# Optimization experiments

Measured on AMD Instinct MI355X. Metric: run time of the kernel, lower is better.

## Reference

```python
import jax, jax.numpy as jnp
import numpy as np

B, V, S, H = 16384, 16, 64, 512


def setup_inputs() -> dict:
    key = jax.random.key(0)
    kx, kw, kb, kws, kbs = jax.random.split(key, 5)
    x = jax.random.normal(kx, (B, V, S), dtype=jnp.float32)
    # per-variable linear layers: weight [V, S, H], bias [V, H]
    W = jax.random.normal(kw, (V, S, H), dtype=jnp.float32) * (1.0 / np.sqrt(S))
    b = jax.random.normal(kb, (V, H), dtype=jnp.float32) * 0.01
    # variable selection linear: hidden -> V
    W_sel = jax.random.normal(kws, (H, V), dtype=jnp.float32) * (1.0 / np.sqrt(H))
    b_sel = jax.random.normal(kbs, (V,), dtype=jnp.float32) * 0.01
    return {"x": x, "W": W, "b": b, "W_sel": W_sel, "b_sel": b_sel}


def reference(x, W, b, W_sel, b_sel):
    # per-variable linears: [B, V, H]
    transformed = jnp.einsum('bvs,vsh->bvh', x, W) + b  # grouped small GEMMs
    # torch stacks to [B, H, V]; mean over variable axis -> [B, H]
    flat = transformed.mean(axis=1)
    # softmax-gated selection weights [B, V] (dropout is identity in eval)
    weights = jax.nn.softmax(flat @ W_sel + b_sel, axis=-1)
    # weighted sum over variables -> [B, H]
    out = jnp.einsum('bvh,bv->bh', transformed, weights)
    return out
```

## Files before the change

kernel.cpp:

```cpp
#include <hip/hip_runtime.h>
#include <hip/hip_bf16.h>
#include <stdint.h>

#define B_ROWS 16384
#define VDIM   16
#define SDIM   64
#define HDIM   512
#define KDIM   1024
#define KP     1056
#define ASTR   1064
#define MROWS  32
#define PLOG_OFF 68096
#define WLDS_OFF (68096 + 8704)
#define K2_LDS   (68096 + 8704 + 2048)

using bf16x8 = __attribute__((ext_vector_type(8))) __bf16;
using u16x8  = __attribute__((ext_vector_type(8))) unsigned short;
using f32x4  = __attribute__((ext_vector_type(4))) float;

__device__ __forceinline__ unsigned short f2bf(float f) {
  unsigned int u = __builtin_bit_cast(unsigned int, f);
  u = (u + 0x7FFFu + ((u >> 16) & 1u)) >> 16;
  return (unsigned short)u;
}
__device__ __forceinline__ float bf2f(unsigned short s) {
  return __builtin_bit_cast(float, (unsigned int)s << 16);
}

__global__ __launch_bounds__(256) void k0_prep(
    const float* __restrict__ W, const float* __restrict__ bias,
    const float* __restrict__ Wsel, const float* __restrict__ bsel,
    unsigned short* __restrict__ Bt, unsigned short* __restrict__ WcombT,
    float* __restrict__ bcomb) {
  __shared__ float bm[HDIM];
  __shared__ float part[16][17];
  __shared__ unsigned short tile[32][264];
  const int t = threadIdx.x;
  if (blockIdx.x < 66) {
    const int k0 = (blockIdx.x >> 1) * 32;
    const int n  = ((blockIdx.x & 1) << 8) + t;
    #pragma unroll 8
    for (int kk = 0; kk < 32; ++kk) {
      const int k = k0 + kk;
      float val;
      if (k < KDIM)            val = W[(size_t)k * HDIM + n];
      else if (k < KDIM + 16)  val = bias[(size_t)(k - KDIM) * HDIM + n];
      else                     val = 0.f;
      tile[kk][t] = f2bf(val);
    }
    __syncthreads();
    unsigned short* dst = Bt + (size_t)n * KP + k0;
    #pragma unroll
    for (int seg = 0; seg < 4; ++seg) {
      unsigned short o[8];
      #pragma unroll
      for (int jj = 0; jj < 8; ++jj) o[jj] = tile[seg * 8 + jj][t];
      *(u16x8*)(dst + seg * 8) = *(const u16x8*)o;
    }
    return;
  }
  const int bid = blockIdx.x - 66;
  if (bid < 256) {
    const int wave = t >> 6, lane = t & 63;
    const int k = bid * 4 + wave;
    const float* wr = W + (size_t)k * HDIM;
    float s[16];
    #pragma unroll
    for (int v = 0; v < 16; ++v) s[v] = 0.f;
    #pragma unroll
    for (int j = 0; j < 8; ++j) {
      const int h = lane + 64 * j;
      const float a = wr[h];
      const float4* wl = (const float4*)(Wsel + h * 16);
      const float4 q0 = wl[0], q1 = wl[1], q2 = wl[2], q3 = wl[3];
      s[0]  = fmaf(a, q0.x, s[0]);  s[1]  = fmaf(a, q0.y, s[1]);
      s[2]  = fmaf(a, q0.z, s[2]);  s[3]  = fmaf(a, q0.w, s[3]);
      s[4]  = fmaf(a, q1.x, s[4]);  s[5]  = fmaf(a, q1.y, s[5]);
      s[6]  = fmaf(a, q1.z, s[6]);  s[7]  = fmaf(a, q1.w, s[7]);
      s[8]  = fmaf(a, q2.x, s[8]);  s[9]  = fmaf(a, q2.y, s[9]);
      s[10] = fmaf(a, q2.z, s[10]); s[11] = fmaf(a, q2.w, s[11]);
      s[12] = fmaf(a, q3.x, s[12]); s[13] = fmaf(a, q3.y, s[13]);
      s[14] = fmaf(a, q3.z, s[14]); s[15] = fmaf(a, q3.w, s[15]);
    }
    #pragma unroll
    for (int off = 32; off > 0; off >>= 1) {
      #pragma unroll
      for (int v = 0; v < 16; ++v) s[v] += __shfl_xor(s[v], off, 64);
    }
    float mine = 0.f;
    #pragma unroll
    for (int v = 0; v < 16; ++v) mine = (lane == v) ? s[v] : mine;
    if (lane < 16) WcombT[lane * KDIM + k] = f2bf(mine * (1.f / 16.f));
  } else {
    for (int h = t; h < HDIM; h += 256) {
      float s = 0.f;
      #pragma unroll
      for (int v = 0; v < VDIM; ++v) s += bias[v * HDIM + h];
      bm[h] = s * (1.f / 16.f);
    }
    __syncthreads();
    int v = t & 15, sl = t >> 4;
    float s = 0.f;
    for (int h = sl * 32; h < sl * 32 + 32; ++h) s = fmaf(bm[h], Wsel[h * VDIM + v], s);
    part[sl][v] = s;
    __syncthreads();
    if (t < 16) {
      float s2 = bsel[t];
      #pragma unroll
      for (int i = 0; i < 16; ++i) s2 += part[i][t];
      bcomb[t] = s2;
    }
  }
}

__global__ __launch_bounds__(512, 4) void k2f_fused(
    const float* __restrict__ x, const unsigned short* __restrict__ WcombT,
    const float* __restrict__ bcomb, const unsigned short* __restrict__ Bt,
    float* __restrict__ C) {
  extern __shared__ unsigned short As[];
  float* plog = (float*)((char*)As + PLOG_OFF);
  float* wlds = (float*)((char*)As + WLDS_OFF);

  const int t = threadIdx.x;
  const int rowb = blockIdx.x * MROWS;
  const int wave = t >> 6, lane = t & 63;
  const int mlane = lane & 15, quad = lane >> 4;

  const int srow = t >> 4;
  const int sc = (t & 15) * 8;
  u16x8 xreg[8];
  {
    const float* xr = x + (size_t)(rowb + srow) * KDIM + sc;
    unsigned short* aw = As + srow * ASTR + sc;
    #pragma unroll
    for (int i = 0; i < 8; ++i) {
      const f32x4 a0 = __builtin_nontemporal_load((const f32x4*)(xr + i * 128));
      const f32x4 a1 = __builtin_nontemporal_load((const f32x4*)(xr + i * 128 + 4));
      u16x8 u;
      u[0] = f2bf(a0[0]); u[1] = f2bf(a0[1]); u[2] = f2bf(a0[2]); u[3] = f2bf(a0[3]);
      u[4] = f2bf(a1[0]); u[5] = f2bf(a1[1]); u[6] = f2bf(a1[2]); u[7] = f2bf(a1[3]);
      xreg[i] = u;
      *(u16x8*)(aw + i * 128) = u;
    }
  }
  __syncthreads();

  {
    const int kh = wave >> 1, rg = wave & 1;
    const unsigned short* al = As + (rg * 16 + mlane) * ASTR + kh * 256 + quad * 8;
    const unsigned short* bl = WcombT + mlane * KDIM + kh * 256 + quad * 8;
    f32x4 acc = {0.f, 0.f, 0.f, 0.f};
    #pragma unroll
    for (int kt = 0; kt < 8; ++kt) {
      bf16x8 a = *(const bf16x8*)al; al += 32;
      bf16x8 b = *(const bf16x8*)bl; bl += 32;
      acc = __builtin_amdgcn_mfma_f32_16x16x32_bf16(a, b, acc, 0, 0, 0);
    }
    float* pl = plog + ((size_t)((kh * 2 + rg) * 16 + quad * 4) * 17 + mlane);
    #pragma unroll
    for (int r = 0; r < 4; ++r) pl[r * 17] = acc[r];
  }
  __syncthreads();

  if (t < 32) {
    const int rg = t >> 4, rr = t & 15;
    float l[16];
    float mx = -1e30f;
    #pragma unroll
    for (int v = 0; v < 16; ++v) {
      float s = bcomb[v];
      #pragma unroll
      for (int kq = 0; kq < 4; ++kq)
        s += plog[((size_t)((kq * 2 + rg) * 16 + rr)) * 17 + v];
      l[v] = s;
      mx = fmaxf(mx, s);
    }
    float s = 0.f;
    #pragma unroll
    for (int v = 0; v < 16; ++v) { l[v] = __expf(l[v] - mx); s += l[v]; }
    const float inv = 1.f / s;
    float* wo = wlds + t * 16;
    #pragma unroll
    for (int v = 0; v < 16; ++v) wo[v] = l[v] * inv;
  }
  __syncthreads();

  {
    float wv[16];
    const f32x4* wq = (const f32x4*)(wlds + srow * 16);
    #pragma unroll
    for (int q = 0; q < 4; ++q) {
      const f32x4 f = wq[q];
      wv[4 * q + 0] = f[0]; wv[4 * q + 1] = f[1];
      wv[4 * q + 2] = f[2]; wv[4 * q + 3] = f[3];
    }
    const int vbase = (t & 15) >> 3;
    unsigned short* aw = As + srow * ASTR + sc;
    #pragma unroll
    for (int i = 0; i < 8; ++i) {
      const float w = wv[2 * i + vbase];
      const u16x8 a = xreg[i];
      u16x8 o;
      #pragma unroll
      for (int j = 0; j < 8; ++j) o[j] = f2bf(w * bf2f(a[j]));
      *(u16x8*)(aw + i * 128) = o;
    }
    if ((t & 15) < 4) {
      const int j8 = (t & 15) * 8;
      unsigned short o[8];
      #pragma unroll
      for (int jj = 0; jj < 8; ++jj)
        o[jj] = (j8 + jj < 16) ? f2bf(wv[j8 + jj]) : (unsigned short)0;
      *(u16x8*)(As + srow * ASTR + KDIM + j8) = *(const u16x8*)o;
    }
  }

  const int colb = wave * 64;
  const unsigned short* bp[4];
  #pragma unroll
  for (int j = 0; j < 4; ++j)
    bp[j] = Bt + (size_t)(colb + j * 16 + mlane) * KP + quad * 8;

  bf16x8 bv0[4], bv1[4];
  #pragma unroll
  for (int j = 0; j < 4; ++j) {
    bv0[j] = *(const bf16x8*)(bp[j]);
    bv1[j] = *(const bf16x8*)(bp[j] + 32);
    bp[j] += 64;
  }

  __syncthreads();

  const unsigned short* ap[2];
  #pragma unroll
  for (int i = 0; i < 2; ++i)
    ap[i] = As + (i * 16 + mlane) * ASTR + quad * 8;

  f32x4 acc[2][4];
  const f32x4 z = {0.f, 0.f, 0.f, 0.f};
  #pragma unroll
  for (int i = 0; i < 2; ++i)
    #pragma unroll
    for (int j = 0; j < 4; ++j) acc[i][j] = z;

  #pragma unroll 1
  for (int kt = 0; kt < 33; ++kt) {
    bf16x8 bnext[4];
    if (kt < 31) {
      #pragma unroll
      for (int j = 0; j < 4; ++j) { bnext[j] = *(const bf16x8*)bp[j]; bp[j] += 32; }
    }
    bf16x8 av[2];
    #pragma unroll
    for (int i = 0; i < 2; ++i) { av[i] = *(const bf16x8*)ap[i]; ap[i] += 32; }
    #pragma unroll
    for (int i = 0; i < 2; ++i)
      #pragma unroll
      for (int j = 0; j < 4; ++j)
        acc[i][j] = __builtin_amdgcn_mfma_f32_16x16x32_bf16(av[i], bv0[j], acc[i][j], 0, 0, 0);
    #pragma unroll
    for (int j = 0; j < 4; ++j) { bv0[j] = bv1[j]; bv1[j] = bnext[j]; }
  }

  #pragma unroll
  for (int i = 0; i < 2; ++i)
    #pragma unroll
    for (int j = 0; j < 4; ++j)
      #pragma unroll
      for (int r = 0; r < 4; ++r) {
        const size_t row = (size_t)rowb + i * 16 + quad * 4 + r;
        const int col = colb + j * 16 + mlane;
        __builtin_nontemporal_store(acc[i][j][r], &C[row * HDIM + col]);
      }
}

extern "C" void kernel_launch(void* const* d_in, const int* in_sizes, int n_in,
                              void* d_out, int out_size, void* d_ws, size_t ws_size,
                              hipStream_t stream) {
  const float* x    = (const float*)d_in[0];
  const float* W    = (const float*)d_in[1];
  const float* bias = (const float*)d_in[2];
  const float* Wsel = (const float*)d_in[3];
  const float* bsel = (const float*)d_in[4];
  float* out = (float*)d_out;

  char* ws = (char*)d_ws;
  unsigned short* Bt     = (unsigned short*)(ws);
  unsigned short* WcombT = (unsigned short*)(ws + 1081344);
  float*          bcomb  = (float*)(ws + 1114112);

  static int lds_set = 0;
  if (!lds_set) {
    hipFuncSetAttribute((const void*)k2f_fused,
                        hipFuncAttributeMaxDynamicSharedMemorySize, K2_LDS);
    lds_set = 1;
  }

  k0_prep<<<323, 256, 0, stream>>>(W, bias, Wsel, bsel, Bt, WcombT, bcomb);
  k2f_fused<<<512, 512, K2_LDS, stream>>>(x, WcombT, bcomb, Bt, out);
}
```

Before: 162.7 us.

## Split gate and GEMM into separate kernels with 64-row double-buffered tiles

```diff
diff --git a/kernel.cpp b/kernel.cpp
--- a/kernel.cpp
+++ b/kernel.cpp
@@ -8,14 +8,18 @@
 #define HDIM   512
 #define KDIM   1024
 #define KP     1056
-#define ASTR   1064
-#define MROWS  32
-#define PLOG_OFF 68096
-#define WLDS_OFF (68096 + 8704)
-#define K2_LDS   (68096 + 8704 + 2048)
+
+#define ASTR     1064
+#define G_PLOG   68096
+#define G_LDS    (68096 + 8704)
+
+#define CSTR     296
+#define BUFU16   (64 * CSTR)
+#define GEMM_LDS (2 * BUFU16 * 2)
 
 using bf16x8 = __attribute__((ext_vector_type(8))) __bf16;
 using u16x8  = __attribute__((ext_vector_type(8))) unsigned short;
+using u16x4  = __attribute__((ext_vector_type(4))) unsigned short;
 using f32x4  = __attribute__((ext_vector_type(4))) float;
 
 __device__ __forceinline__ unsigned short f2bf(float f) {
@@ -113,33 +117,29 @@
   }
 }
 
-__global__ __launch_bounds__(512, 4) void k2f_fused(
+__global__ __launch_bounds__(512, 4) void k1_gate(
     const float* __restrict__ x, const unsigned short* __restrict__ WcombT,
-    const float* __restrict__ bcomb, const unsigned short* __restrict__ Bt,
-    float* __restrict__ C) {
+    const float* __restrict__ bcomb, float* __restrict__ wgate) {
   extern __shared__ unsigned short As[];
-  float* plog = (float*)((char*)As + PLOG_OFF);
-  float* wlds = (float*)((char*)As + WLDS_OFF);
+  float* plog = (float*)((char*)As + G_PLOG);
 
   const int t = threadIdx.x;
-  const int rowb = blockIdx.x * MROWS;
+  const int rowb = blockIdx.x * 32;
   const int wave = t >> 6, lane = t & 63;
   const int mlane = lane & 15, quad = lane >> 4;
 
-  const int srow = t >> 4;
-  const int sc = (t & 15) * 8;
-  u16x8 xreg[8];
   {
+    const int srow = t >> 4;
+    const int sc = (t & 15) * 8;
     const float* xr = x + (size_t)(rowb + srow) * KDIM + sc;
     unsigned short* aw = As + srow * ASTR + sc;
     #pragma unroll
     for (int i = 0; i < 8; ++i) {
-      const f32x4 a0 = __builtin_nontemporal_load((const f32x4*)(xr + i * 128));
-      const f32x4 a1 = __builtin_nontemporal_load((const f32x4*)(xr + i * 128 + 4));
+      const float4 a0 = *(const float4*)(xr + i * 128);
+      const float4 a1 = *(const float4*)(xr + i * 128 + 4);
       u16x8 u;
-      u[0] = f2bf(a0[0]); u[1] = f2bf(a0[1]); u[2] = f2bf(a0[2]); u[3] = f2bf(a0[3]);
-      u[4] = f2bf(a1[0]); u[5] = f2bf(a1[1]); u[6] = f2bf(a1[2]); u[7] = f2bf(a1[3]);
-      xreg[i] = u;
+      u[0] = f2bf(a0.x); u[1] = f2bf(a0.y); u[2] = f2bf(a0.z); u[3] = f2bf(a0.w);
+      u[4] = f2bf(a1.x); u[5] = f2bf(a1.y); u[6] = f2bf(a1.z); u[7] = f2bf(a1.w);
       *(u16x8*)(aw + i * 128) = u;
     }
   }
@@ -179,48 +179,57 @@
     #pragma unroll
     for (int v = 0; v < 16; ++v) { l[v] = __expf(l[v] - mx); s += l[v]; }
     const float inv = 1.f / s;
-    float* wo = wlds + t * 16;
-    #pragma unroll
-    for (int v = 0; v < 16; ++v) wo[v] = l[v] * inv;
-  }
-  __syncthreads();
-
+    float* wo = wgate + (size_t)(rowb + t) * 16;
+    #pragma unroll
+    for (int q = 0; q < 4; ++q) {
+      f32x4 o = {l[4*q] * inv, l[4*q+1] * inv, l[4*q+2] * inv, l[4*q+3] * inv};
+      *(f32x4*)(wo + 4 * q) = o;
+    }
+  }
+}
+
+__global__ __launch_bounds__(512, 2) void k2_gemm(
+    const float* __restrict__ x, const float* __restrict__ wgate,
+    const unsigned short* __restrict__ Bt, float* __restrict__ C) {
+  extern __shared__ unsigned short As[];
+  const int t = threadIdx.x;
+  const int rowb = blockIdx.x * 64;
+  const int wave = t >> 6, lane = t & 63;
+  const int mlane = lane & 15, quad = lane >> 4;
+
+  const int srow = t >> 3;
+  const int sk   = (t & 7) * 32;
+  const float* xrow = x + (size_t)(rowb + srow) * KDIM + sk;
+  const float* wrow = wgate + (size_t)(rowb + srow) * 16;
+  const int vsub = (t & 7) >> 1;
+  const float w0 = wrow[vsub], w1 = wrow[4 + vsub],
+              w2 = wrow[8 + vsub], w3 = wrow[12 + vsub];
+
+  unsigned short* myA0 = As + srow * CSTR + sk;
+
+  f32x4 xr[8];
+  #pragma unroll
+  for (int i = 0; i < 8; ++i) xr[i] = *(const f32x4*)(xrow + i * 4);
   {
-    float wv[16];
-    const f32x4* wq = (const f32x4*)(wlds + srow * 16);
-    #pragma unroll
-    for (int q = 0; q < 4; ++q) {
-      const f32x4 f = wq[q];
-      wv[4 * q + 0] = f[0]; wv[4 * q + 1] = f[1];
-      wv[4 * q + 2] = f[2]; wv[4 * q + 3] = f[3];
-    }
-    const int vbase = (t & 15) >> 3;
-    unsigned short* aw = As + srow * ASTR + sc;
-    #pragma unroll
-    for (int i = 0; i < 8; ++i) {
-      const float w = wv[2 * i + vbase];
-      const u16x8 a = xreg[i];
+    #pragma unroll
+    for (int s = 0; s < 4; ++s) {
+      const f32x4 a = xr[2 * s], b2 = xr[2 * s + 1];
       u16x8 o;
-      #pragma unroll
-      for (int j = 0; j < 8; ++j) o[j] = f2bf(w * bf2f(a[j]));
-      *(u16x8*)(aw + i * 128) = o;
-    }
-    if ((t & 15) < 4) {
-      const int j8 = (t & 15) * 8;
-      unsigned short o[8];
-      #pragma unroll
-      for (int jj = 0; jj < 8; ++jj)
-        o[jj] = (j8 + jj < 16) ? f2bf(wv[j8 + jj]) : (unsigned short)0;
-      *(u16x8*)(As + srow * ASTR + KDIM + j8) = *(const u16x8*)o;
-    }
-  }
+      o[0] = f2bf(w0 * a[0]);  o[1] = f2bf(w0 * a[1]);
+      o[2] = f2bf(w0 * a[2]);  o[3] = f2bf(w0 * a[3]);
+      o[4] = f2bf(w0 * b2[0]); o[5] = f2bf(w0 * b2[1]);
+      o[6] = f2bf(w0 * b2[2]); o[7] = f2bf(w0 * b2[3]);
+      *(u16x8*)(myA0 + s * 8) = o;
+    }
+  }
+  #pragma unroll
+  for (int i = 0; i < 8; ++i) xr[i] = *(const f32x4*)(xrow + 256 + i * 4);
 
   const int colb = wave * 64;
   const unsigned short* bp[4];
   #pragma unroll
   for (int j = 0; j < 4; ++j)
     bp[j] = Bt + (size_t)(colb + j * 16 + mlane) * KP + quad * 8;
-
   bf16x8 bv0[4], bv1[4];
   #pragma unroll
   for (int j = 0; j < 4; ++j) {
@@ -231,39 +240,73 @@
 
   __syncthreads();
 
-  const unsigned short* ap[2];
-  #pragma unroll
-  for (int i = 0; i < 2; ++i)
-    ap[i] = As + (i * 16 + mlane) * ASTR + quad * 8;
-
-  f32x4 acc[2][4];
+  f32x4 acc[4][4];
   const f32x4 z = {0.f, 0.f, 0.f, 0.f};
   #pragma unroll
-  for (int i = 0; i < 2; ++i)
+  for (int i = 0; i < 4; ++i)
     #pragma unroll
     for (int j = 0; j < 4; ++j) acc[i][j] = z;
 
+  int ktg = 0;
   #pragma unroll 1
-  for (int kt = 0; kt < 33; ++kt) {
-    bf16x8 bnext[4];
-    if (kt < 31) {
-      #pragma unroll
-      for (int j = 0; j < 4; ++j) { bnext[j] = *(const bf16x8*)bp[j]; bp[j] += 32; }
-    }
-    bf16x8 av[2];
-    #pragma unroll
-    for (int i = 0; i < 2; ++i) { av[i] = *(const bf16x8*)ap[i]; ap[i] += 32; }
-    #pragma unroll
-    for (int i = 0; i < 2; ++i)
-      #pragma unroll
-      for (int j = 0; j < 4; ++j)
-        acc[i][j] = __builtin_amdgcn_mfma_f32_16x16x32_bf16(av[i], bv0[j], acc[i][j], 0, 0, 0);
-    #pragma unroll
-    for (int j = 0; j < 4; ++j) { bv0[j] = bv1[j]; bv1[j] = bnext[j]; }
-  }
-
-  #pragma unroll
-  for (int i = 0; i < 2; ++i)
+  for (int c = 0; c < 5; ++c) {
+    const unsigned short* buf = As + (c & 1) * BUFU16;
+    const int nkt = (c < 4) ? 8 : 1;
+    #pragma unroll 1
+    for (int kt = 0; kt < nkt; ++kt) {
+      bf16x8 bnext[4];
+      if (ktg < 31) {
+        #pragma unroll
+        for (int j = 0; j < 4; ++j) { bnext[j] = *(const bf16x8*)bp[j]; bp[j] += 32; }
+      }
+      bf16x8 av[4];
+      #pragma unroll
+      for (int i = 0; i < 4; ++i)
+        av[i] = *(const bf16x8*)(buf + (i * 16 + mlane) * CSTR + kt * 32 + quad * 8);
+      #pragma unroll
+      for (int i = 0; i < 4; ++i)
+        #pragma unroll
+        for (int j = 0; j < 4; ++j)
+          acc[i][j] = __builtin_amdgcn_mfma_f32_16x16x32_bf16(av[i], bv0[j], acc[i][j], 0, 0, 0);
+      #pragma unroll
+      for (int j = 0; j < 4; ++j) { bv0[j] = bv1[j]; bv1[j] = bnext[j]; }
+      ++ktg;
+    }
+    if (c < 3) {
+      unsigned short* dst = As + ((c + 1) & 1) * BUFU16 + srow * CSTR + sk;
+      const float ws = (c == 0) ? w1 : (c == 1) ? w2 : w3;
+      #pragma unroll
+      for (int s = 0; s < 4; ++s) {
+        const f32x4 a = xr[2 * s], b2 = xr[2 * s + 1];
+        u16x8 o;
+        o[0] = f2bf(ws * a[0]);  o[1] = f2bf(ws * a[1]);
+        o[2] = f2bf(ws * a[2]);  o[3] = f2bf(ws * a[3]);
+        o[4] = f2bf(ws * b2[0]); o[5] = f2bf(ws * b2[1]);
+        o[6] = f2bf(ws * b2[2]); o[7] = f2bf(ws * b2[3]);
+        *(u16x8*)(dst + s * 8) = o;
+      }
+      if (c < 2) {
+        #pragma unroll
+        for (int i = 0; i < 8; ++i)
+          xr[i] = *(const f32x4*)(xrow + (c + 2) * 256 + i * 4);
+      }
+      __syncthreads();
+    } else if (c == 3) {
+      const int j4 = (t & 7) * 4;
+      u16x4 o;
+      if (j4 < 16) {
+        const f32x4 wv = *(const f32x4*)(wgate + (size_t)(rowb + srow) * 16 + j4);
+        o[0] = f2bf(wv[0]); o[1] = f2bf(wv[1]); o[2] = f2bf(wv[2]); o[3] = f2bf(wv[3]);
+      } else {
+        o[0] = 0; o[1] = 0; o[2] = 0; o[3] = 0;
+      }
+      *(u16x4*)(As + srow * CSTR + j4) = o;
+      __syncthreads();
+    }
+  }
+
+  #pragma unroll
+  for (int i = 0; i < 4; ++i)
     #pragma unroll
     for (int j = 0; j < 4; ++j)
       #pragma unroll
@@ -288,14 +331,18 @@
   unsigned short* Bt     = (unsigned short*)(ws);
   unsigned short* WcombT = (unsigned short*)(ws + 1081344);
   float*          bcomb  = (float*)(ws + 1114112);
+  float*          wgate  = (float*)(ws + 1114368);
 
   static int lds_set = 0;
   if (!lds_set) {
-    hipFuncSetAttribute((const void*)k2f_fused,
-                        hipFuncAttributeMaxDynamicSharedMemorySize, K2_LDS);
+    hipFuncSetAttribute((const void*)k1_gate,
+                        hipFuncAttributeMaxDynamicSharedMemorySize, G_LDS);
+    hipFuncSetAttribute((const void*)k2_gemm,
+                        hipFuncAttributeMaxDynamicSharedMemorySize, GEMM_LDS);
     lds_set = 1;
   }
 
   k0_prep<<<323, 256, 0, stream>>>(W, bias, Wsel, bsel, Bt, WcombT, bcomb);
-  k2f_fused<<<512, 512, K2_LDS, stream>>>(x, WcombT, bcomb, Bt, out);
-}
+  k1_gate<<<512, 512, G_LDS, stream>>>(x, WcombT, bcomb, wgate);
+  k2_gemm<<<256, 512, GEMM_LDS, stream>>>(x, wgate, Bt, out);
+}
```

New measurement: 161.1 us. About the same (-1.0%).

## Split fused kernel into gate pass and LDS-tiled 128x128 GEMM

Applied to the files above, without the earlier changes.

```diff
diff --git a/kernel.cpp b/kernel.cpp
--- a/kernel.cpp
+++ b/kernel.cpp
@@ -7,12 +7,12 @@
 #define SDIM   64
 #define HDIM   512
 #define KDIM   1024
-#define KP     1056
-#define ASTR   1064
-#define MROWS  32
-#define PLOG_OFF 68096
-#define WLDS_OFF (68096 + 8704)
-#define K2_LDS   (68096 + 8704 + 2048)
+#define KP2    1088
+
+#define ASTR     1064
+#define G_PLOG   68096
+#define G_WLDS   (68096 + 8704)
+#define G_LDS    (68096 + 8704 + 2048)
 
 using bf16x8 = __attribute__((ext_vector_type(8))) __bf16;
 using u16x8  = __attribute__((ext_vector_type(8))) unsigned short;
@@ -25,6 +25,13 @@
 }
 __device__ __forceinline__ float bf2f(unsigned short s) {
   return __builtin_bit_cast(float, (unsigned int)s << 16);
+}
+
+__device__ __forceinline__ void gl_lds16(const void* g, void* l) {
+  __builtin_amdgcn_global_load_lds(
+      (const __attribute__((address_space(1))) unsigned int*)(uintptr_t)g,
+      (__attribute__((address_space(3))) unsigned int*)(unsigned int)(uintptr_t)l,
+      16, 0, 0);
 }
 
 __global__ __launch_bounds__(256) void k0_prep(
@@ -36,7 +43,7 @@
   __shared__ float part[16][17];
   __shared__ unsigned short tile[32][264];
   const int t = threadIdx.x;
-  if (blockIdx.x < 66) {
+  if (blockIdx.x < 68) {
     const int k0 = (blockIdx.x >> 1) * 32;
     const int n  = ((blockIdx.x & 1) << 8) + t;
     #pragma unroll 8
@@ -49,7 +56,7 @@
       tile[kk][t] = f2bf(val);
     }
     __syncthreads();
-    unsigned short* dst = Bt + (size_t)n * KP + k0;
+    unsigned short* dst = Bt + (size_t)n * KP2 + k0;
     #pragma unroll
     for (int seg = 0; seg < 4; ++seg) {
       unsigned short o[8];
@@ -59,7 +66,7 @@
     }
     return;
   }
-  const int bid = blockIdx.x - 66;
+  const int bid = blockIdx.x - 68;
   if (bid < 256) {
     const int wave = t >> 6, lane = t & 63;
     const int k = bid * 4 + wave;
@@ -113,24 +120,25 @@
   }
 }
 
-__global__ __launch_bounds__(512, 4) void k2f_fused(
+__global__ __launch_bounds__(512, 4) void k1_gate(
     const float* __restrict__ x, const unsigned short* __restrict__ WcombT,
-    const float* __restrict__ bcomb, const unsigned short* __restrict__ Bt,
-    float* __restrict__ C) {
+    const float* __restrict__ bcomb, unsigned short* __restrict__ Ap,
+    int rowbase) {
   extern __shared__ unsigned short As[];
-  float* plog = (float*)((char*)As + PLOG_OFF);
-  float* wlds = (float*)((char*)As + WLDS_OFF);
+  float* plog = (float*)((char*)As + G_PLOG);
+  float* wlds = (float*)((char*)As + G_WLDS);
 
   const int t = threadIdx.x;
-  const int rowb = blockIdx.x * MROWS;
+  const int lrow0 = blockIdx.x * 32;
+  const int grow0 = rowbase + lrow0;
   const int wave = t >> 6, lane = t & 63;
   const int mlane = lane & 15, quad = lane >> 4;
-
   const int srow = t >> 4;
   const int sc = (t & 15) * 8;
+
   u16x8 xreg[8];
   {
-    const float* xr = x + (size_t)(rowb + srow) * KDIM + sc;
+    const float* xr = x + (size_t)(grow0 + srow) * KDIM + sc;
     unsigned short* aw = As + srow * ASTR + sc;
     #pragma unroll
     for (int i = 0; i < 8; ++i) {
@@ -195,7 +203,7 @@
       wv[4 * q + 2] = f[2]; wv[4 * q + 3] = f[3];
     }
     const int vbase = (t & 15) >> 3;
-    unsigned short* aw = As + srow * ASTR + sc;
+    unsigned short* aw = Ap + (size_t)(lrow0 + srow) * KP2 + sc;
     #pragma unroll
     for (int i = 0; i < 8; ++i) {
       const float w = wv[2 * i + vbase];
@@ -205,72 +213,92 @@
       for (int j = 0; j < 8; ++j) o[j] = f2bf(w * bf2f(a[j]));
       *(u16x8*)(aw + i * 128) = o;
     }
-    if ((t & 15) < 4) {
-      const int j8 = (t & 15) * 8;
-      unsigned short o[8];
-      #pragma unroll
-      for (int jj = 0; jj < 8; ++jj)
-        o[jj] = (j8 + jj < 16) ? f2bf(wv[j8 + jj]) : (unsigned short)0;
-      *(u16x8*)(As + srow * ASTR + KDIM + j8) = *(const u16x8*)o;
-    }
-  }
-
-  const int colb = wave * 64;
-  const unsigned short* bp[4];
+    const int seg = t & 15;
+    if (seg < 8) {
+      u16x8 o;
+      #pragma unroll
+      for (int jj = 0; jj < 8; ++jj) {
+        const int c = seg * 8 + jj;
+        o[jj] = (c < 16) ? f2bf(wv[c]) : (unsigned short)0;
+      }
+      *(u16x8*)(Ap + (size_t)(lrow0 + srow) * KP2 + KDIM + seg * 8) = o;
+    }
+  }
+}
+
+__global__ __launch_bounds__(256) void k2_gemm(
+    const unsigned short* __restrict__ Ap, const unsigned short* __restrict__ Bt,
+    float* __restrict__ C, int rowbase) {
+  __shared__ unsigned short As[8192];
+  __shared__ unsigned short Bs[8192];
+
+  const int t = threadIdx.x;
+  const int nwg = gridDim.x;
+  const int q = nwg >> 3, r = nwg & 7;
+  const int xcd = blockIdx.x & 7, idx = blockIdx.x >> 3;
+  const int bid = (xcd < r ? xcd * (q + 1) : r * (q + 1) + (xcd - r) * q) + idx;
+
+  const int lrowb = (bid >> 2) * 128;
+  const int colb  = (bid & 3) * 128;
+  const int wave = t >> 6, lane = t & 63;
+  const int mlane = lane & 15, quad = lane >> 4;
+  const int wr = wave >> 1, wc = wave & 1;
+
+  const int l8 = lane >> 3, lk = (lane & 7) * 8;
+  const unsigned short* asrc[4];
+  const unsigned short* bsrc[4];
   #pragma unroll
-  for (int j = 0; j < 4; ++j)
-    bp[j] = Bt + (size_t)(colb + j * 16 + mlane) * KP + quad * 8;
-
-  bf16x8 bv0[4], bv1[4];
-  #pragma unroll
-  for (int j = 0; j < 4; ++j) {
-    bv0[j] = *(const bf16x8*)(bp[j]);
-    bv1[j] = *(const bf16x8*)(bp[j] + 32);
-    bp[j] += 64;
-  }
-
-  __syncthreads();
-
-  const unsigned short* ap[2];
-  #pragma unroll
-  for (int i = 0; i < 2; ++i)
-    ap[i] = As + (i * 16 + mlane) * ASTR + quad * 8;
-
-  f32x4 acc[2][4];
+  for (int i = 0; i < 4; ++i) {
+    asrc[i] = Ap + (size_t)(lrowb + wave * 32 + i * 8 + l8) * KP2 + lk;
+    bsrc[i] = Bt + (size_t)(colb + wave * 32 + i * 8 + l8) * KP2 + lk;
+  }
+  unsigned short* adst = As + wave * 2048;
+  unsigned short* bdst = Bs + wave * 2048;
+
+  f32x4 acc[4][4];
   const f32x4 z = {0.f, 0.f, 0.f, 0.f};
   #pragma unroll
-  for (int i = 0; i < 2; ++i)
+  for (int i = 0; i < 4; ++i)
     #pragma unroll
     for (int j = 0; j < 4; ++j) acc[i][j] = z;
 
   #pragma unroll 1
-  for (int kt = 0; kt < 33; ++kt) {
-    bf16x8 bnext[4];
-    if (kt < 31) {
-      #pragma unroll
-      for (int j = 0; j < 4; ++j) { bnext[j] = *(const bf16x8*)bp[j]; bp[j] += 32; }
-    }
-    bf16x8 av[2];
-    #pragma unroll
-    for (int i = 0; i < 2; ++i) { av[i] = *(const bf16x8*)ap[i]; ap[i] += 32; }
-    #pragma unroll
-    for (int i = 0; i < 2; ++i)
+  for (int kt = 0; kt < 17; ++kt) {
+    #pragma unroll
+    for (int i = 0; i < 4; ++i) gl_lds16(asrc[i], adst + i * 512);
+    #pragma unroll
+    for (int i = 0; i < 4; ++i) gl_lds16(bsrc[i], bdst + i * 512);
+    #pragma unroll
+    for (int i = 0; i < 4; ++i) { asrc[i] += 64; bsrc[i] += 64; }
+    __syncthreads();
+
+    #pragma unroll
+    for (int ks = 0; ks < 2; ++ks) {
+      bf16x8 av[4], bv[4];
+      #pragma unroll
+      for (int i = 0; i < 4; ++i)
+        av[i] = *(const bf16x8*)(As + (wr * 64 + i * 16 + mlane) * 64 + ks * 32 + quad * 8);
       #pragma unroll
       for (int j = 0; j < 4; ++j)
-        acc[i][j] = __builtin_amdgcn_mfma_f32_16x16x32_bf16(av[i], bv0[j], acc[i][j], 0, 0, 0);
-    #pragma unroll
-    for (int j = 0; j < 4; ++j) { bv0[j] = bv1[j]; bv1[j] = bnext[j]; }
+        bv[j] = *(const bf16x8*)(Bs + (wc * 64 + j * 16 + mlane) * 64 + ks * 32 + quad * 8);
+      #pragma unroll
+      for (int i = 0; i < 4; ++i)
+        #pragma unroll
+        for (int j = 0; j < 4; ++j)
+          acc[i][j] = __builtin_amdgcn_mfma_f32_16x16x32_bf16(av[i], bv[j], acc[i][j], 0, 0, 0);
+    }
+    __syncthreads();
   }
 
   #pragma unroll
-  for (int i = 0; i < 2; ++i)
+  for (int i = 0; i < 4; ++i)
     #pragma unroll
     for (int j = 0; j < 4; ++j)
       #pragma unroll
-      for (int r = 0; r < 4; ++r) {
-        const size_t row = (size_t)rowb + i * 16 + quad * 4 + r;
-        const int col = colb + j * 16 + mlane;
-        __builtin_nontemporal_store(acc[i][j][r], &C[row * HDIM + col]);
+      for (int r2 = 0; r2 < 4; ++r2) {
+        const size_t row = (size_t)rowbase + lrowb + wr * 64 + i * 16 + quad * 4 + r2;
+        const int col = colb + wc * 64 + j * 16 + mlane;
+        __builtin_nontemporal_store(acc[i][j][r2], &C[row * HDIM + col]);
       }
 }
 
@@ -286,16 +314,28 @@
 
   char* ws = (char*)d_ws;
   unsigned short* Bt     = (unsigned short*)(ws);
-  unsigned short* WcombT = (unsigned short*)(ws + 1081344);
-  float*          bcomb  = (float*)(ws + 1114112);
+  unsigned short* WcombT = (unsigned short*)(ws + 1114112);
+  float*          bcomb  = (float*)(ws + 1146880);
+  unsigned short* Ap     = (unsigned short*)(ws + 1147136);
+
+  const size_t fixed = 1147136;
+  size_t avail = (ws_size > fixed) ? (ws_size - fixed) : 0;
+  size_t maxRows = avail / (KP2 * 2);
+  int sliceRows = (int)((maxRows / 128) * 128);
+  if (sliceRows > B_ROWS) sliceRows = B_ROWS;
+  if (sliceRows < 128) sliceRows = 128;
 
   static int lds_set = 0;
   if (!lds_set) {
-    hipFuncSetAttribute((const void*)k2f_fused,
-                        hipFuncAttributeMaxDynamicSharedMemorySize, K2_LDS);
+    hipFuncSetAttribute((const void*)k1_gate,
+                        hipFuncAttributeMaxDynamicSharedMemorySize, G_LDS);
     lds_set = 1;
   }
 
-  k0_prep<<<323, 256, 0, stream>>>(W, bias, Wsel, bsel, Bt, WcombT, bcomb);
-  k2f_fused<<<512, 512, K2_LDS, stream>>>(x, WcombT, bcomb, Bt, out);
-}
+  k0_prep<<<325, 256, 0, stream>>>(W, bias, Wsel, bsel, Bt, WcombT, bcomb);
+  for (int r0 = 0; r0 < B_ROWS; r0 += sliceRows) {
+    const int rows = (B_ROWS - r0 < sliceRows) ? (B_ROWS - r0) : sliceRows;
+    k1_gate<<<rows / 32, 512, G_LDS, stream>>>(x, WcombT, bcomb, Ap, r0);
+    k2_gemm<<<(rows / 128) * 4, 256, 0, stream>>>(Ap, Bt, out, r0);
+  }
+}
```

Result: no change. 165.5 us (+1.7%).
